# Performance work log

Hardware: AMD Instinct MI355X
Metric: run time of the kernel (lower is better)

Reference implementation:

```python
import jax, jax.numpy as jnp
import numpy as np

G = 16          # avg_pool_output_size (grid side after adaptive pool)
PATCH = 2       # patch_size
HIDDEN = 256
NOUT = 128


def setup_inputs() -> dict:
    key = jax.random.key(0)
    ks = jax.random.split(key, 7)
    B, C, H, W = 8, 32, 32, 32
    D = C * PATCH * PATCH + 2          # 130 (patch pixels + 2 coords)
    IN0 = 2 * D                        # 260 (pair concat)
    s = 0.02
    return {
        "x": jax.random.normal(ks[0], (B, C, H, W), jnp.float32),
        "W0": jax.random.normal(ks[1], (IN0, HIDDEN), jnp.float32) * s,
        "b0": jax.random.normal(ks[2], (HIDDEN,), jnp.float32) * s,
        "W1": jax.random.normal(ks[3], (HIDDEN, HIDDEN), jnp.float32) * s,
        "b1": jax.random.normal(ks[4], (HIDDEN,), jnp.float32) * s,
        "Wout": jax.random.normal(ks[5], (HIDDEN, NOUT), jnp.float32) * s,
        "bout": jax.random.normal(ks[6], (NOUT,), jnp.float32) * s,
    }


def _patch_node_features(x):
    """x: [B,C,H,W] -> node features [B, P, C*p^2 + 2] (patch pixels + coords)."""
    b, c, h, w = x.shape
    # adaptive avg pool to GxG (evenly divisible case == block mean)
    pooled = x.reshape(b, c, G, h // G, G, w // G).mean(axis=(3, 5))  # [B,C,G,G]
    flat = pooled.reshape(b, c, G * G)
    Pg = G - PATCH + 1                          # patches per side (15)
    P = Pg * Pg                                 # 225 nodes
    ri = jnp.arange(Pg)
    ki = jnp.arange(PATCH)
    # flat pixel index (r+ki)*G + (q+kj), patch order row-major, pixel order row-major
    row = (ri[:, None, None, None] + ki[None, None, :, None])  # [Pg,1,p,1]
    col = (ri[None, :, None, None] + ki[None, None, None, :])  # [1,Pg,1,p]
    pix = (row * G + col).reshape(P, PATCH * PATCH)            # [P, p^2]
    feats = flat[:, :, pix]                                    # [B,C,P,p^2]
    # torch: [b,c,P,p2] -> permute -> [b,c,p2,P] -> reshape [b,c*p2,P] -> [b,P,c*p2]
    feats = feats.transpose(0, 2, 1, 3).reshape(b, P, c * PATCH * PATCH)
    # spatial coordinates: (x=col, y=row) centered by int(sqrt(P)/2)
    cx = jnp.broadcast_to(jnp.arange(Pg)[None, :], (Pg, Pg))
    cy = jnp.broadcast_to(jnp.arange(Pg)[:, None], (Pg, Pg))
    coord = jnp.stack([cx, cy], axis=-1).reshape(P, 2).astype(feats.dtype) - (Pg // 2)
    coord = jnp.broadcast_to(coord[None], (b, P, 2))
    return jnp.concatenate([feats, coord], axis=2)             # [B,P,D]


def reference(x, W0, b0, W1, b1, Wout, bout):
    feats = _patch_node_features(x)          # [B,P,D]
    b, P, D = feats.shape
    # pair tensor: cat([x_i, x_j]) with x_i[b,i,j]=feats[b,j], x_j[b,i,j]=feats[b,i]
    pair = jnp.concatenate([
        jnp.broadcast_to(feats[:, None, :, :], (b, P, P, D)),
        jnp.broadcast_to(feats[:, :, None, :], (b, P, P, D)),
    ], axis=-1).reshape(b, P * P, 2 * D)     # [B, P^2, 2D]
    out = jax.nn.leaky_relu(pair @ W0 + b0)  # [B,P^2,H]
    out = jax.nn.leaky_relu(out @ W1 + b1)
    out = out.mean(axis=1)                   # [B,H]
    return out @ Wout + bout                 # [B,NOUT]
```

## Files before the change

kernel.cpp:

```cpp
#include <hip/hip_runtime.h>
#include <hip/hip_bf16.h>
#include <stdint.h>

#define NB 8
#define NP 225
#define PGRID 15
#define DH 256
#define DIN 130

typedef _Float16 f16x8 __attribute__((ext_vector_type(8)));
typedef float    f32x4 __attribute__((ext_vector_type(4)));

static __device__ __forceinline__ float lrelu(float x) { return fmaxf(x, 0.01f * x); }

__global__ void prep_kernel(const float* __restrict__ x, const float* __restrict__ W0,
                            const float* __restrict__ b0, const float* __restrict__ W1,
                            _Float16* __restrict__ U, _Float16* __restrict__ V,
                            _Float16* __restrict__ W1F, float* __restrict__ accg) {
    int blk = blockIdx.x;
    if (blk >= 360) {
        int t = (blk - 360) * 256 + threadIdx.x;
        int slot = t >> 6, l = t & 63;
        int nf = slot >> 3, ks = slot & 7;
        int n = nf * 16 + (l & 15);
        int kb = l >> 4;
        f16x8 wv;
        #pragma unroll
        for (int e = 0; e < 8; ++e) {
            int k = ks * 32 + kb * 8 + e;
            wv[e] = (_Float16)W1[k * DH + n];
        }
        reinterpret_cast<f16x8*>(W1F)[t] = wv;
        return;
    }
    int bb = blk / 45;
    int p0 = (blk % 45) * 5;
    if (blk % 45 == 0) accg[bb * DH + threadIdx.x] = 0.0f;
    __shared__ float fl[5][DIN];
    int t = threadIdx.x;
    for (int idx = t; idx < 5 * DIN; idx += 256) {
        int pp = idx / DIN, f = idx % DIN;
        int p = p0 + pp;
        int r = p / PGRID, c = p % PGRID;
        float val;
        if (f < 128) {
            int ch = f >> 2, q = f & 3, ki = q >> 1, kj = q & 1;
            int R = r + ki, C = c + kj;
            const float* xp = x + (((size_t)bb * 32 + ch) * 32 + 2 * R) * 32 + 2 * C;
            val = 0.25f * (xp[0] + xp[1] + xp[32] + xp[33]);
        } else {
            val = (f == 128) ? (float)(c - 7) : (float)(r - 7);
        }
        fl[pp][f] = val;
    }
    __syncthreads();
    int n = t;
    float u[5] = {0, 0, 0, 0, 0}, v[5] = {0, 0, 0, 0, 0};
    for (int k = 0; k < DIN; ++k) {
        float wa = W0[k * DH + n];
        float wb = W0[(DIN + k) * DH + n];
        #pragma unroll
        for (int pp = 0; pp < 5; ++pp) {
            float f = fl[pp][k];
            u[pp] = fmaf(f, wa, u[pp]);
            v[pp] = fmaf(f, wb, v[pp]);
        }
    }
    float bb0 = b0[n];
    #pragma unroll
    for (int pp = 0; pp < 5; ++pp) {
        size_t base = ((size_t)bb * NP + p0 + pp) * DH + n;
        U[base] = (_Float16)(u[pp] + bb0);
        V[base] = (_Float16)v[pp];
    }
}

__global__ __launch_bounds__(256, 2) void main_kernel(
        const _Float16* __restrict__ U, const _Float16* __restrict__ V,
        const _Float16* __restrict__ W1F, const float* __restrict__ b1,
        float* __restrict__ accg) {
    __shared__ f16x8 Af[2048];
    __shared__ _Float16 Upad[16 * 264];
    const int JT = 15, CHUNKS = 9, TILESPC = 7;
    int blk = blockIdx.x;
    int bb = blk / (JT * CHUNKS);
    int rem = blk % (JT * CHUNKS);
    int jt = rem / CHUNKS, ch = rem % CHUNKS;
    int j0 = jt * 16;
    int tile0 = ch * TILESPC;
    int nt = min(TILESPC, 57 - tile0);
    int t = threadIdx.x, l = t & 63, w = t >> 6;

    {
        int jj = t >> 4, kk = (t & 15) * 16;
        int jc = j0 + jj; if (jc >= NP) jc = NP - 1;
        const f16x8* src = reinterpret_cast<const f16x8*>(U + ((size_t)bb * NP + jc) * DH + kk);
        *reinterpret_cast<f16x8*>(&Upad[jj * 264 + kk])     = src[0];
        *reinterpret_cast<f16x8*>(&Upad[jj * 264 + kk + 8]) = src[1];
    }
    f16x8 bv[4][8];
    const f16x8* Bp = reinterpret_cast<const f16x8*>(W1F);
    #pragma unroll
    for (int nf = 0; nf < 4; ++nf)
        #pragma unroll
        for (int ks = 0; ks < 8; ++ks)
            bv[nf][ks] = Bp[((w * 4 + nf) * 8 + ks) * 64 + l];
    float b1v[4];
    #pragma unroll
    for (int nf = 0; nf < 4; ++nf) b1v[nf] = b1[w * 64 + nf * 16 + (l & 15)];
    float psum[4] = {0.f, 0.f, 0.f, 0.f};
    int kb = l >> 4;
    const _Float16* Urow = &Upad[(l & 15) * 264 + kb * 8];
    __syncthreads();

    for (int itl = 0; itl < nt; ++itl) {
        int i0 = (tile0 + itl) * 4;
        int ii = i0 + w;
        int ic = ii < NP ? ii : NP - 1;
        const f16x8* Vrow = reinterpret_cast<const f16x8*>(V + ((size_t)bb * NP + ic) * DH);
        if (itl) __syncthreads();

        #pragma unroll
        for (int ks = 0; ks < 8; ++ks) {
            f16x8 uv = *reinterpret_cast<const f16x8*>(Urow + ks * 32);
            f16x8 vv = Vrow[ks * 4 + kb];
            f16x8 s  = uv + vv;
            f16x8 a  = __builtin_elementwise_max(s, s * (_Float16)0.01f);
            Af[(w * 8 + ks) * 64 + l] = a;
        }
        __syncthreads();

        f32x4 acc[4][4];
        #pragma unroll
        for (int mf = 0; mf < 4; ++mf)
            #pragma unroll
            for (int nf = 0; nf < 4; ++nf)
                acc[mf][nf] = (f32x4){b1v[nf], b1v[nf], b1v[nf], b1v[nf]};
        #pragma unroll
        for (int ks = 0; ks < 8; ++ks) {
            f16x8 av[4];
            #pragma unroll
            for (int mf = 0; mf < 4; ++mf) av[mf] = Af[(mf * 8 + ks) * 64 + l];
            #pragma unroll
            for (int mf = 0; mf < 4; ++mf)
                #pragma unroll
                for (int nf = 0; nf < 4; ++nf)
                    acc[mf][nf] = __builtin_amdgcn_mfma_f32_16x16x32_f16(
                        av[mf], bv[nf][ks], acc[mf][nf], 0, 0, 0);
        }

        int rowg = l >> 4;
        #pragma unroll
        for (int mf = 0; mf < 4; ++mf) {
            bool iv = (i0 + mf) < NP;
            #pragma unroll
            for (int r = 0; r < 4; ++r) {
                bool valid = iv && ((j0 + rowg * 4 + r) < NP);
                #pragma unroll
                for (int nf = 0; nf < 4; ++nf) {
                    float h = lrelu(acc[mf][nf][r]);
                    psum[nf] += valid ? h : 0.f;
                }
            }
        }
    }

    #pragma unroll
    for (int nf = 0; nf < 4; ++nf) {
        psum[nf] += __shfl_xor(psum[nf], 16);
        psum[nf] += __shfl_xor(psum[nf], 32);
    }
    if (l < 16) {
        #pragma unroll
        for (int nf = 0; nf < 4; ++nf)
            atomicAdd(&accg[bb * DH + w * 64 + nf * 16 + l], psum[nf]);
    }
}

__global__ void out_kernel(const float* __restrict__ accg, const float* __restrict__ Wout,
                           const float* __restrict__ bout, float* __restrict__ out) {
    int bb = blockIdx.x;
    int o = threadIdx.x;
    float s = 0.f;
    for (int n = 0; n < DH; ++n)
        s = fmaf(accg[bb * DH + n], Wout[n * 128 + o], s);
    out[bb * 128 + o] = s * (1.0f / 50625.0f) + bout[o];
}

extern "C" void kernel_launch(void* const* d_in, const int* in_sizes, int n_in,
                              void* d_out, int out_size, void* d_ws, size_t ws_size,
                              hipStream_t stream) {
    const float* x    = (const float*)d_in[0];
    const float* W0   = (const float*)d_in[1];
    const float* b0   = (const float*)d_in[2];
    const float* W1   = (const float*)d_in[3];
    const float* b1   = (const float*)d_in[4];
    const float* Wout = (const float*)d_in[5];
    const float* bout = (const float*)d_in[6];
    float* out = (float*)d_out;

    char* ws = (char*)d_ws;
    _Float16* U    = (_Float16*)(ws);
    _Float16* V    = (_Float16*)(ws + 921600);
    _Float16* W1F  = (_Float16*)(ws + 2 * 921600);
    float*    accg = (float*)(ws + 2 * 921600 + 131072);

    prep_kernel<<<392, 256, 0, stream>>>(x, W0, b0, W1, U, V, W1F, accg);
    main_kernel<<<NB * 15 * 9, 256, 0, stream>>>(U, V, W1F, b1, accg);
    out_kernel<<<NB, 128, 0, stream>>>(accg, Wout, bout, out);
}
```

Measured before the change: 92.56 us.

## Warp-specialize main kernel into producer and MFMA consumer waves with double buffering

Block size doubles to 512 threads. Four producer waves build the leaky-ReLU(U+V) A-tile into a double-buffered LDS slot while four consumer waves run MFMAs on the previous tile, so A-tile construction overlaps with matrix work. The grid shrinks from 1080 to 240 blocks, each handling about 28 tiles, which amortizes the U/W1 register loads over more work and issues fewer atomics. The cost is fewer blocks in flight on a large GPU, half the waves doing only light ALU work, and one block-wide barrier per tile.

```diff
diff --git a/kernel.cpp b/kernel.cpp
--- a/kernel.cpp
+++ b/kernel.cpp
@@ -75,105 +75,125 @@
     }
 }
 
-__global__ __launch_bounds__(256, 2) void main_kernel(
+__global__ __launch_bounds__(512, 2) void main_kernel(
         const _Float16* __restrict__ U, const _Float16* __restrict__ V,
         const _Float16* __restrict__ W1F, const float* __restrict__ b1,
         float* __restrict__ accg) {
-    __shared__ f16x8 Af[2048];
+    __shared__ f16x8 Af[2][2048];
     __shared__ _Float16 Upad[16 * 264];
-    const int JT = 15, CHUNKS = 9, TILESPC = 7;
+    const int JT = 15, CHUNKS = 2;
     int blk = blockIdx.x;
     int bb = blk / (JT * CHUNKS);
     int rem = blk % (JT * CHUNKS);
     int jt = rem / CHUNKS, ch = rem % CHUNKS;
     int j0 = jt * 16;
-    int tile0 = ch * TILESPC;
-    int nt = min(TILESPC, 57 - tile0);
+    int tile0 = ch * 29;
+    int nt = ch ? 28 : 29;
     int t = threadIdx.x, l = t & 63, w = t >> 6;
+    bool producer = (w < 4);
+    int pw = w & 3;
 
     {
-        int jj = t >> 4, kk = (t & 15) * 16;
+        int jj = t >> 5, kk = (t & 31) * 8;
         int jc = j0 + jj; if (jc >= NP) jc = NP - 1;
-        const f16x8* src = reinterpret_cast<const f16x8*>(U + ((size_t)bb * NP + jc) * DH + kk);
-        *reinterpret_cast<f16x8*>(&Upad[jj * 264 + kk])     = src[0];
-        *reinterpret_cast<f16x8*>(&Upad[jj * 264 + kk + 8]) = src[1];
-    }
-    f16x8 bv[4][8];
-    const f16x8* Bp = reinterpret_cast<const f16x8*>(W1F);
-    #pragma unroll
-    for (int nf = 0; nf < 4; ++nf)
-        #pragma unroll
-        for (int ks = 0; ks < 8; ++ks)
-            bv[nf][ks] = Bp[((w * 4 + nf) * 8 + ks) * 64 + l];
-    float b1v[4];
-    #pragma unroll
-    for (int nf = 0; nf < 4; ++nf) b1v[nf] = b1[w * 64 + nf * 16 + (l & 15)];
-    float psum[4] = {0.f, 0.f, 0.f, 0.f};
+        *reinterpret_cast<f16x8*>(&Upad[jj * 264 + kk]) =
+            *reinterpret_cast<const f16x8*>(U + ((size_t)bb * NP + jc) * DH + kk);
+    }
+
     int kb = l >> 4;
     const _Float16* Urow = &Upad[(l & 15) * 264 + kb * 8];
+    const _Float16* Vbb = V + (size_t)bb * NP * DH;
+
+    f16x8 bv[4][8];
+    float b1v[4] = {0, 0, 0, 0};
+    float jmask[4] = {0, 0, 0, 0};
+    float psum[4] = {0.f, 0.f, 0.f, 0.f};
+    if (!producer) {
+        const f16x8* Bp = reinterpret_cast<const f16x8*>(W1F);
+        #pragma unroll
+        for (int nf = 0; nf < 4; ++nf)
+            #pragma unroll
+            for (int ks = 0; ks < 8; ++ks)
+                bv[nf][ks] = Bp[((pw * 4 + nf) * 8 + ks) * 64 + l];
+        #pragma unroll
+        for (int nf = 0; nf < 4; ++nf) b1v[nf] = b1[pw * 64 + nf * 16 + (l & 15)];
+        int rowg = l >> 4;
+        #pragma unroll
+        for (int r = 0; r < 4; ++r) jmask[r] = (j0 + rowg * 4 + r) < NP ? 1.0f : 0.0f;
+    }
     __syncthreads();
 
-    for (int itl = 0; itl < nt; ++itl) {
-        int i0 = (tile0 + itl) * 4;
-        int ii = i0 + w;
-        int ic = ii < NP ? ii : NP - 1;
-        const f16x8* Vrow = reinterpret_cast<const f16x8*>(V + ((size_t)bb * NP + ic) * DH);
-        if (itl) __syncthreads();
-
+    auto build = [&](int itl2, int bufi) {
+        int ic = (tile0 + itl2) * 4 + pw; if (ic >= NP) ic = NP - 1;
+        const _Float16* Vr = Vbb + (size_t)ic * DH + kb * 8;
         #pragma unroll
         for (int ks = 0; ks < 8; ++ks) {
             f16x8 uv = *reinterpret_cast<const f16x8*>(Urow + ks * 32);
-            f16x8 vv = Vrow[ks * 4 + kb];
+            f16x8 vv = *reinterpret_cast<const f16x8*>(Vr + ks * 32);
             f16x8 s  = uv + vv;
             f16x8 a  = __builtin_elementwise_max(s, s * (_Float16)0.01f);
-            Af[(w * 8 + ks) * 64 + l] = a;
-        }
-        __syncthreads();
-
-        f32x4 acc[4][4];
-        #pragma unroll
-        for (int mf = 0; mf < 4; ++mf)
-            #pragma unroll
-            for (int nf = 0; nf < 4; ++nf)
-                acc[mf][nf] = (f32x4){b1v[nf], b1v[nf], b1v[nf], b1v[nf]};
-        #pragma unroll
-        for (int ks = 0; ks < 8; ++ks) {
-            f16x8 av[4];
-            #pragma unroll
-            for (int mf = 0; mf < 4; ++mf) av[mf] = Af[(mf * 8 + ks) * 64 + l];
+            Af[bufi][(pw * 8 + ks) * 64 + l] = a;
+        }
+    };
+
+    if (producer) build(0, 0);
+    __syncthreads();
+    int cur = 0;
+
+    for (int itl = 0; itl < nt; ++itl) {
+        if (producer) {
+            if (itl + 1 < nt) build(itl + 1, cur ^ 1);
+        } else {
+            int i0 = (tile0 + itl) * 4;
+            f32x4 acc[4][4];
             #pragma unroll
             for (int mf = 0; mf < 4; ++mf)
                 #pragma unroll
                 for (int nf = 0; nf < 4; ++nf)
-                    acc[mf][nf] = __builtin_amdgcn_mfma_f32_16x16x32_f16(
-                        av[mf], bv[nf][ks], acc[mf][nf], 0, 0, 0);
-        }
-
-        int rowg = l >> 4;
-        #pragma unroll
-        for (int mf = 0; mf < 4; ++mf) {
-            bool iv = (i0 + mf) < NP;
-            #pragma unroll
-            for (int r = 0; r < 4; ++r) {
-                bool valid = iv && ((j0 + rowg * 4 + r) < NP);
+                    acc[mf][nf] = (f32x4){b1v[nf], b1v[nf], b1v[nf], b1v[nf]};
+            #pragma unroll
+            for (int ks = 0; ks < 8; ++ks) {
+                f16x8 av[4];
                 #pragma unroll
-                for (int nf = 0; nf < 4; ++nf) {
-                    float h = lrelu(acc[mf][nf][r]);
-                    psum[nf] += valid ? h : 0.f;
+                for (int mf = 0; mf < 4; ++mf)
+                    av[mf] = Af[cur][(mf * 8 + ks) * 64 + l];
+                #pragma unroll
+                for (int mf = 0; mf < 4; ++mf)
+                    #pragma unroll
+                    for (int nf = 0; nf < 4; ++nf)
+                        acc[mf][nf] = __builtin_amdgcn_mfma_f32_16x16x32_f16(
+                            av[mf], bv[nf][ks], acc[mf][nf], 0, 0, 0);
+            }
+            #pragma unroll
+            for (int mf = 0; mf < 4; ++mf) {
+                if (i0 + mf < NP) {
+                    #pragma unroll
+                    for (int r = 0; r < 4; ++r) {
+                        #pragma unroll
+                        for (int nf = 0; nf < 4; ++nf) {
+                            float a = acc[mf][nf][r];
+                            float h = fmaxf(a, 0.01f * a);
+                            psum[nf] = fmaf(h, jmask[r], psum[nf]);
+                        }
+                    }
                 }
             }
         }
-    }
-
-    #pragma unroll
-    for (int nf = 0; nf < 4; ++nf) {
-        psum[nf] += __shfl_xor(psum[nf], 16);
-        psum[nf] += __shfl_xor(psum[nf], 32);
-    }
-    if (l < 16) {
-        #pragma unroll
-        for (int nf = 0; nf < 4; ++nf)
-            atomicAdd(&accg[bb * DH + w * 64 + nf * 16 + l], psum[nf]);
+        __syncthreads();
+        cur ^= 1;
+    }
+
+    if (!producer) {
+        #pragma unroll
+        for (int nf = 0; nf < 4; ++nf) {
+            psum[nf] += __shfl_xor(psum[nf], 16);
+            psum[nf] += __shfl_xor(psum[nf], 32);
+        }
+        if (l < 16) {
+            #pragma unroll
+            for (int nf = 0; nf < 4; ++nf)
+                atomicAdd(&accg[bb * DH + pw * 64 + nf * 16 + l], psum[nf]);
+        }
     }
 }
 
@@ -206,6 +226,6 @@
     float*    accg = (float*)(ws + 2 * 921600 + 131072);
 
     prep_kernel<<<392, 256, 0, stream>>>(x, W0, b0, W1, U, V, W1F, accg);
-    main_kernel<<<NB * 15 * 9, 256, 0, stream>>>(U, V, W1F, b1, accg);
+    main_kernel<<<NB * 15 * 2, 512, 0, stream>>>(U, V, W1F, b1, accg);
     out_kernel<<<NB, 128, 0, stream>>>(accg, Wout, bout, out);
 }
```

Result: slower. 102.1 us (+10.3%).
